# Optimization experiments

Hardware: AMD Instinct MI355X
Metric: run time of the kernel (lower is better)

## Reference

```python
import jax, jax.numpy as jnp
import numpy as np

N_NODES = 10000
N_EDGES = 320000
D = 256
L = 3
BN_EPS = 1e-5


def _segment_softmax(logits, seg, num_segments):
    # numerically stable softmax over variable-sized segments (incoming edges per node)
    m = jax.ops.segment_max(logits, seg, num_segments=num_segments)
    e = jnp.exp(logits - m[seg])
    s = jax.ops.segment_sum(e, seg, num_segments=num_segments)
    return e / s[seg]


def setup_inputs() -> dict:
    key = jax.random.key(0)
    ks = jax.random.split(key, 20)
    scale = 1.0 / np.sqrt(D)
    inp = {
        "x": jax.random.normal(ks[0], (N_NODES, D), dtype=jnp.float32),
        "edge_index": jax.random.randint(ks[1], (2, N_EDGES), 0, N_NODES, dtype=jnp.int64),
        # TransformerConv params (heads=1, concat=False)
        "Wq": jax.random.normal(ks[2], (D, D), jnp.float32) * scale,
        "bq": jnp.zeros((D,), jnp.float32),
        "Wk": jax.random.normal(ks[3], (D, D), jnp.float32) * scale,
        "bk": jnp.zeros((D,), jnp.float32),
        "Wv": jax.random.normal(ks[4], (D, D), jnp.float32) * scale,
        "bv": jnp.zeros((D,), jnp.float32),
        "Ws": jax.random.normal(ks[5], (D, D), jnp.float32) * scale,  # lin_skip (root weight)
        "bs": jnp.zeros((D,), jnp.float32),
        # SAGEConv params per layer: lin_l (neighbors, with bias), lin_r (root, no bias)
        "Wl": jax.random.normal(ks[6], (L, D, D), jnp.float32) * scale,
        "bl": jnp.zeros((L, D), jnp.float32),
        "Wr": jax.random.normal(ks[7], (L, D, D), jnp.float32) * scale,
        # BatchNorm affine params (eval mode: running_mean=0, running_var=1)
        "gamma": jnp.ones((L, D), jnp.float32) + 0.1 * jax.random.normal(ks[8], (L, D), jnp.float32),
        "beta": 0.1 * jax.random.normal(ks[9], (L, D), jnp.float32),
        # residual gate parameter (scalar)
        "alpha_res": jnp.asarray(0.5, jnp.float32),
    }
    return inp


def reference(x, edge_index, Wq, bq, Wk, bk, Wv, bv, Ws, bs, Wl, bl, Wr, gamma, beta, alpha_res):
    src, dst = edge_index[0], edge_index[1]  # message j -> i
    n, d = x.shape

    # ---- TransformerConv (heads=1, concat=False, eval: no dropout) ----
    q = x @ Wq + bq
    k = x @ Wk + bk
    v = x @ Wv + bv
    logits = jnp.sum(q[dst] * k[src], axis=-1) / jnp.sqrt(jnp.asarray(d, x.dtype))  # [E]
    attn = _segment_softmax(logits, dst, n)  # [E]
    agg = jax.ops.segment_sum(attn[:, None] * v[src], dst, num_segments=n)  # [N,D]
    h = agg + x @ Ws + bs  # root/skip connection
    h = jax.nn.relu(h)

    # in-degree for SAGE mean aggregation
    deg = jax.ops.segment_sum(jnp.ones((src.shape[0],), x.dtype), dst, num_segments=n)
    deg = jnp.maximum(deg, 1.0)[:, None]

    prev = h
    bn_scale = 1.0 / jnp.sqrt(1.0 + BN_EPS)  # eval-mode BN with running stats (0, 1)
    al = jax.nn.sigmoid(alpha_res)
    for i in range(Wl.shape[0]):
        mean_nb = jax.ops.segment_sum(h[src], dst, num_segments=n) / deg  # gather-mean-scatter
        z = mean_nb @ Wl[i] + bl[i] + h @ Wr[i]
        z = z * bn_scale * gamma[i] + beta[i]
        z = al * z + (1.0 - al) * prev
        h = jax.nn.relu(z)
        prev = h
    return h
```

## Files before the change

kernel.cpp:

```cpp
#include <hip/hip_runtime.h>
#include <hip/hip_bf16.h>

typedef unsigned short u16;
typedef unsigned int u32;
typedef unsigned char u8;
typedef __bf16 bf16x8 __attribute__((ext_vector_type(8)));
typedef float f32x4 __attribute__((ext_vector_type(4)));
typedef float f32x2 __attribute__((ext_vector_type(2)));

#define DIM 256
#define BN_SCALE 0.9999950000374997f

__device__ __forceinline__ float bf2f(u16 u) {
    union { unsigned u; float f; } c; c.u = ((unsigned)u) << 16; return c.f;
}
__device__ __forceinline__ u16 f2bf(float f) {
    union { float f; unsigned u; } c; c.f = f;
    unsigned u = c.u;
    unsigned r = (u + 0x7FFFu + ((u >> 16) & 1u)) >> 16;
    return (u16)r;
}
__device__ __forceinline__ float asf(unsigned u) {
    union { unsigned u; float f; } c; c.u = u; return c.f;
}
__device__ __forceinline__ void cvt8(int4 v, float* f) {
    unsigned a0 = (unsigned)v.x, a1 = (unsigned)v.y, a2 = (unsigned)v.z, a3 = (unsigned)v.w;
    f[0] = asf(a0 << 16); f[1] = asf(a0 & 0xFFFF0000u);
    f[2] = asf(a1 << 16); f[3] = asf(a1 & 0xFFFF0000u);
    f[4] = asf(a2 << 16); f[5] = asf(a2 & 0xFFFF0000u);
    f[6] = asf(a3 << 16); f[7] = asf(a3 & 0xFFFF0000u);
}
__device__ __forceinline__ void dec4(unsigned u, float* f) {
    f32x2 lo = __builtin_amdgcn_cvt_pk_f32_fp8((int)u, false);
    f32x2 hi = __builtin_amdgcn_cvt_pk_f32_fp8((int)u, true);
    f[0] = lo.x; f[1] = lo.y; f[2] = hi.x; f[3] = hi.y;
}
__device__ __forceinline__ unsigned pack4(float a, float b, float c, float d) {
    int u = __builtin_amdgcn_cvt_pk_fp8_f32(a, b, 0, false);
    u = __builtin_amdgcn_cvt_pk_fp8_f32(c, d, u, true);
    return (unsigned)u;
}
__device__ __forceinline__ void gl_lds16(const u16* g, u16* l) {
    __builtin_amdgcn_global_load_lds(
        (__attribute__((address_space(1))) const u32*)(const void*)g,
        (__attribute__((address_space(3))) u32*)(void*)l, 16, 0, 0);
}

__global__ void k_detect(const u16* __restrict__ xu, const long long* __restrict__ e64,
                         int* __restrict__ flags) {
    int lane = threadIdx.x;
    int plausible = 0;
#pragma unroll
    for (int j = 0; j < 4; ++j) {
        u16 u = xu[lane * 4 + j];
        int ex = (u >> 7) & 0xFF;
        plausible += (u == 0 || (ex >= 115 && ex <= 131)) ? 1 : 0;
    }
#pragma unroll
    for (int o = 32; o; o >>= 1) plausible += __shfl_xor(plausible, o, 64);
    long long hi = e64[lane] >> 32;
    unsigned long long b = __ballot(hi == 0);
    if (lane == 0) {
        flags[0] = (plausible >= 200) ? 1 : 0;
        flags[1] = (b == ~0ULL) ? 1 : 0;
    }
}

struct CvtDesc {
    const void* src[15];
    int cum[16];
};
__global__ void k_convert(CvtDesc d, const int* __restrict__ flags,
                          u16* __restrict__ arena, int total) {
    int i = blockIdx.x * 256 + threadIdx.x;
    if (i >= total) return;
    int t = 0;
    while (i >= d.cum[t + 1]) ++t;
    int j = i - d.cum[t];
    u16 v;
    if (flags[0]) v = ((const u16*)d.src[t])[j];
    else          v = f2bf(((const float*)d.src[t])[j]);
    arena[i] = v;
}

struct TDesc { const u16* src[12]; u16* dst[12]; };
__global__ __launch_bounds__(256) void k_transpose(TDesc td) {
    __shared__ u16 t[64][72];
    int m = blockIdx.x >> 4, tl = blockIdx.x & 15;
    int tr = (tl >> 2) * 64, tc = (tl & 3) * 64;
    const u16* S = td.src[m];
    u16* D = td.dst[m];
    int r = threadIdx.x >> 2, cs = (threadIdx.x & 3) * 16;
    *(int4*)&t[r][cs]     = *(const int4*)&S[(tr + r) * 256 + tc + cs];
    *(int4*)&t[r][cs + 8] = *(const int4*)&S[(tr + r) * 256 + tc + cs + 8];
    __syncthreads();
    u16 tmp[16];
#pragma unroll
    for (int j = 0; j < 16; ++j) tmp[j] = t[cs + j][r];
    *(int4*)&D[(tc + r) * 256 + tr + cs]     = *(int4*)&tmp[0];
    *(int4*)&D[(tc + r) * 256 + tr + cs + 8] = *(int4*)&tmp[8];
}

__global__ void k_edges(const int* __restrict__ ei32, const int* __restrict__ flags,
                        int* __restrict__ srcN, int* __restrict__ dstN,
                        int* __restrict__ deg, int E) {
    int e = blockIdx.x * 256 + threadIdx.x;
    if (e >= E) return;
    const long long* ei64 = (const long long*)ei32;
    int w64 = flags[1];
    int s = w64 ? (int)ei64[e]     : ei32[e];
    int d = w64 ? (int)ei64[E + e] : ei32[E + e];
    srcN[e] = s; dstN[e] = d;
    atomicAdd(&deg[d], 1);
}

__global__ __launch_bounds__(1024) void k_scan(const int* __restrict__ deg,
                                               int* __restrict__ offs,
                                               int* __restrict__ cursor, int N, int E) {
    __shared__ int s[1024];
    int t = threadIdx.x;
    int P = (N + 1023) >> 10;
    int base = t * P;
    int run = 0;
    for (int j = 0; j < P; ++j) { int idx = base + j; if (idx < N) run += deg[idx]; }
    s[t] = run;
    __syncthreads();
    int total = run;
    for (int off = 1; off < 1024; off <<= 1) {
        int v = 0;
        if (t >= off) v = s[t - off];
        __syncthreads();
        if (t >= off) s[t] += v;
        __syncthreads();
    }
    int r = s[t] - total;
    for (int j = 0; j < P; ++j) {
        int idx = base + j;
        if (idx < N) { offs[idx] = r; cursor[idx] = r; r += deg[idx]; }
    }
    if (t == 0) offs[N] = E;
}

__global__ void k_fill(const int* __restrict__ srcN, const int* __restrict__ dstN,
                       int* __restrict__ cursor, int* __restrict__ csr, int E) {
    int e = blockIdx.x * 256 + threadIdx.x;
    if (e < E) {
        int d = dstN[e];
        int pos = atomicAdd(&cursor[d], 1);
        csr[pos] = srcN[e];
    }
}

__global__ __launch_bounds__(256) void gemm_qkvs(
    const u16* __restrict__ x, const u16* __restrict__ WT,
    const u16* __restrict__ bias, u16* __restrict__ out, int M) {
    __shared__ __align__(16) u16 lds[16384];
    u16* As = lds;
    u16* Bs = lds + 8192;
    int tid = threadIdx.x, w = tid >> 6, lane = tid & 63;
    int l15 = lane & 15, quad = lane >> 4;
    int lr = lane >> 3, lc = lane & 7;
    int bm0 = blockIdx.x * 128, bn0 = blockIdx.y * 128;
    f32x4 acc[4][4];
#pragma unroll
    for (int a = 0; a < 4; ++a)
#pragma unroll
        for (int b = 0; b < 4; ++b) acc[a][b] = (f32x4){0.f, 0.f, 0.f, 0.f};

    for (int k0 = 0; k0 < 256; k0 += 64) {
#pragma unroll
        for (int j = 0; j < 4; ++j) {
            int ar = (w * 4 + j) * 8 + lr;
            int grow = bm0 + ar; if (grow >= M) grow = M - 1;
            gl_lds16(x + (size_t)grow * 256 + k0 + lc * 8, &As[(w * 4 + j) * 512]);
        }
#pragma unroll
        for (int j = 0; j < 4; ++j) {
            int nr = (w * 4 + j) * 8 + lr;
            gl_lds16(WT + (size_t)(bn0 + nr) * 256 + k0 + lc * 8, &Bs[(w * 4 + j) * 512]);
        }
        __syncthreads();
        int wm = w & 1, wn = w >> 1;
#pragma unroll
        for (int s = 0; s < 2; ++s) {
            bf16x8 a[4], b[4];
#pragma unroll
            for (int t = 0; t < 4; ++t)
                a[t] = *(const bf16x8*)&As[(wm * 64 + t * 16 + l15) * 64 + s * 32 + quad * 8];
#pragma unroll
            for (int t = 0; t < 4; ++t)
                b[t] = *(const bf16x8*)&Bs[(wn * 64 + t * 16 + l15) * 64 + s * 32 + quad * 8];
#pragma unroll
            for (int rt = 0; rt < 4; ++rt)
#pragma unroll
                for (int ct = 0; ct < 4; ++ct)
                    acc[rt][ct] = __builtin_amdgcn_mfma_f32_16x16x32_bf16(a[rt], b[ct], acc[rt][ct], 0, 0, 0);
        }
        __syncthreads();
    }
    int wm = w & 1, wn = w >> 1;
    u16* oL = lds + w * 4096;
#pragma unroll
    for (int rt = 0; rt < 4; ++rt)
#pragma unroll
        for (int ct = 0; ct < 4; ++ct) {
            int col = bn0 + wn * 64 + ct * 16 + l15;
            float bv = bf2f(bias[col]);
#pragma unroll
            for (int r = 0; r < 4; ++r)
                oL[(rt * 16 + quad * 4 + r) * 64 + ct * 16 + l15] = f2bf(acc[rt][ct][r] + bv);
        }
    __syncthreads();
#pragma unroll
    for (int j = 0; j < 8; ++j) {
        int orow = j * 8 + lr;
        int grow = bm0 + wm * 64 + orow;
        if (grow < M)
            *(int4*)&out[(size_t)grow * 1024 + bn0 + wn * 64 + lc * 8] = *(const int4*)&oL[orow * 64 + lc * 8];
    }
}

__global__ void k_pack8(const u16* __restrict__ qkvs, u8* __restrict__ kv8, int N) {
    int t = blockIdx.x * 256 + threadIdx.x;
    if (t >= N * 64) return;
    int i = t >> 6, s = t & 63;
    int4 v = *(const int4*)(qkvs + (size_t)i * 1024 + 256 + s * 8);
    float f[8]; cvt8(v, f);
    uint2 o;
    o.x = pack4(f[0], f[1], f[2], f[3]);
    o.y = pack4(f[4], f[5], f[6], f[7]);
    *(uint2*)(kv8 + (size_t)i * 512 + s * 8) = o;
}

__global__ __launch_bounds__(256) void k_attn(const u16* __restrict__ qkvs,
                                              const u8* __restrict__ kv8,
                                              const int* __restrict__ csr,
                                              const int* __restrict__ offs,
                                              u16* __restrict__ hb,
                                              u8* __restrict__ h8, int N) {
    int wv = threadIdx.x >> 6, lane = threadIdx.x & 63;
    int i = blockIdx.x * 4 + wv;
    if (i >= N) return;
    int sub = lane & 7;
    int e8 = lane >> 3;
    size_t row = (size_t)i * 1024;

    float qf[32];
    {
        const u16* qp = qkvs + row + sub * 32;
#pragma unroll
        for (int j = 0; j < 4; ++j) {
            int4 v = *(const int4*)(qp + j * 8);
            float t[8]; cvt8(v, t);
#pragma unroll
            for (int d = 0; d < 8; ++d) qf[j * 8 + d] = t[d] * 0.0625f;
        }
    }
    int e0 = offs[i], e1 = offs[i + 1];
    float m = -1e30f, denom = 0.f;
    float acc[32];
#pragma unroll
    for (int j = 0; j < 32; ++j) acc[j] = 0.f;

    for (int base = e0; base < e1; base += 8) {
        int e = base + e8;
        int sidx = csr[(e < e1) ? e : (e1 - 1)];
        const u8* kp = kv8 + (size_t)sidx * 512 + sub * 32;
        uint4 ka = *(const uint4*)kp;
        uint4 kb = *(const uint4*)(kp + 16);
        uint4 va = *(const uint4*)(kp + 256);
        uint4 vb = *(const uint4*)(kp + 272);
        unsigned kw[8] = {ka.x, ka.y, ka.z, ka.w, kb.x, kb.y, kb.z, kb.w};
        float p = 0.f;
#pragma unroll
        for (int j = 0; j < 8; ++j) {
            float t[4]; dec4(kw[j], t);
            p += qf[j * 4] * t[0] + qf[j * 4 + 1] * t[1] + qf[j * 4 + 2] * t[2] + qf[j * 4 + 3] * t[3];
        }
        p += __shfl_xor(p, 1, 64);
        p += __shfl_xor(p, 2, 64);
        p += __shfl_xor(p, 4, 64);
        if (e >= e1) p = -1e30f;
        float pm = p;
        pm = fmaxf(pm, __shfl_xor(pm, 8, 64));
        pm = fmaxf(pm, __shfl_xor(pm, 16, 64));
        pm = fmaxf(pm, __shfl_xor(pm, 32, 64));
        if (pm > m) {
            float sc = __expf(m - pm);
            denom *= sc;
#pragma unroll
            for (int j = 0; j < 32; ++j) acc[j] *= sc;
            m = pm;
        }
        float w = __expf(p - m);
        denom += w;
        unsigned vw[8] = {va.x, va.y, va.z, va.w, vb.x, vb.y, vb.z, vb.w};
#pragma unroll
        for (int j = 0; j < 8; ++j) {
            float t[4]; dec4(vw[j], t);
            acc[j * 4]     += w * t[0];
            acc[j * 4 + 1] += w * t[1];
            acc[j * 4 + 2] += w * t[2];
            acc[j * 4 + 3] += w * t[3];
        }
    }
    denom += __shfl_xor(denom, 8, 64);
    denom += __shfl_xor(denom, 16, 64);
    denom += __shfl_xor(denom, 32, 64);
    float inv = (denom > 0.f) ? 1.f / denom : 0.f;
#pragma unroll
    for (int j = 0; j < 32; ++j) {
        acc[j] += __shfl_xor(acc[j], 8, 64);
        acc[j] += __shfl_xor(acc[j], 16, 64);
        acc[j] += __shfl_xor(acc[j], 32, 64);
    }
    if (e8 == 0) {
        const u16* skp = qkvs + row + 768 + sub * 32;
        float h[32];
#pragma unroll
        for (int j = 0; j < 4; ++j) {
            int4 sv = *(const int4*)(skp + j * 8);
            float t[8]; cvt8(sv, t);
            u16 o[8];
#pragma unroll
            for (int d = 0; d < 8; ++d) {
                float hv = fmaxf(acc[j * 8 + d] * inv + t[d], 0.f);
                h[j * 8 + d] = hv;
                o[d] = f2bf(hv);
            }
            *(int4*)(hb + (size_t)i * 256 + sub * 32 + j * 8) = *(const int4*)o;
        }
        uint4 p0, p1;
        p0.x = pack4(h[0], h[1], h[2], h[3]);   p0.y = pack4(h[4], h[5], h[6], h[7]);
        p0.z = pack4(h[8], h[9], h[10], h[11]); p0.w = pack4(h[12], h[13], h[14], h[15]);
        p1.x = pack4(h[16], h[17], h[18], h[19]); p1.y = pack4(h[20], h[21], h[22], h[23]);
        p1.z = pack4(h[24], h[25], h[26], h[27]); p1.w = pack4(h[28], h[29], h[30], h[31]);
        *(uint4*)(h8 + (size_t)i * 256 + sub * 32) = p0;
        *(uint4*)(h8 + (size_t)i * 256 + sub * 32 + 16) = p1;
    }
}

__global__ __launch_bounds__(256) void k_agg(const u8* __restrict__ h8,
                                             const int* __restrict__ csr,
                                             const int* __restrict__ offs,
                                             u16* __restrict__ mean_out, int N) {
    int half = threadIdx.x >> 5, hl = threadIdx.x & 31;
    int i = blockIdx.x * 8 + half;
    if (i >= N) return;
    int e0 = offs[i], e1 = offs[i + 1];
    const u8* base = h8 + (unsigned)hl * 8;
    float acc[8];
#pragma unroll
    for (int d = 0; d < 8; ++d) acc[d] = 0.f;
    int e = e0;
    for (; e + 8 <= e1; e += 8) {
        uint2 r[8];
#pragma unroll
        for (int j = 0; j < 8; ++j)
            r[j] = *(const uint2*)(base + (size_t)csr[e + j] * 256);
#pragma unroll
        for (int j = 0; j < 8; ++j) {
            float f0[4], f1[4];
            dec4(r[j].x, f0); dec4(r[j].y, f1);
            acc[0] += f0[0]; acc[1] += f0[1]; acc[2] += f0[2]; acc[3] += f0[3];
            acc[4] += f1[0]; acc[5] += f1[1]; acc[6] += f1[2]; acc[7] += f1[3];
        }
    }
    for (; e < e1; ++e) {
        uint2 r0 = *(const uint2*)(base + (size_t)csr[e] * 256);
        float f0[4], f1[4];
        dec4(r0.x, f0); dec4(r0.y, f1);
        acc[0] += f0[0]; acc[1] += f0[1]; acc[2] += f0[2]; acc[3] += f0[3];
        acc[4] += f1[0]; acc[5] += f1[1]; acc[6] += f1[2]; acc[7] += f1[3];
    }
    int dg = e1 - e0; if (dg < 1) dg = 1;
    float inv = 1.f / (float)dg;
    u16 o16[8];
#pragma unroll
    for (int d = 0; d < 8; ++d) o16[d] = f2bf(acc[d] * inv);
    *(int4*)(mean_out + (size_t)i * 256 + (unsigned)hl * 8) = *(const int4*)o16;
}

__global__ __launch_bounds__(256) void gemm_sage(
    const u16* __restrict__ meanA, const u16* __restrict__ hin,
    const u16* __restrict__ WlT, const u16* __restrict__ WrT,
    const u16* __restrict__ bl, const u16* __restrict__ gamma,
    const u16* __restrict__ beta, const u16* __restrict__ alpha,
    u16* __restrict__ hout, u8* __restrict__ h8out, float* __restrict__ fout, int M) {
    __shared__ __align__(16) u16 lds[12288];
    u16* As = lds;
    u16* Bs = lds + 8192;
    int tid = threadIdx.x, w = tid >> 6, lane = tid & 63;
    int l15 = lane & 15, quad = lane >> 4;
    int lr = lane >> 3, lc = lane & 7;
    int bm0 = blockIdx.x * 128, n0 = blockIdx.y * 64;
    f32x4 acc[2][4];
#pragma unroll
    for (int a = 0; a < 2; ++a)
#pragma unroll
        for (int b = 0; b < 4; ++b) acc[a][b] = (f32x4){0.f, 0.f, 0.f, 0.f};

    for (int k0 = 0; k0 < 512; k0 += 64) {
        const u16* Asrc = (k0 < 256) ? meanA : hin;
        const u16* Bsrc = (k0 < 256) ? WlT : WrT;
        int kc = k0 & 255;
#pragma unroll
        for (int j = 0; j < 4; ++j) {
            int ar = (w * 4 + j) * 8 + lr;
            int grow = bm0 + ar; if (grow >= M) grow = M - 1;
            gl_lds16(Asrc + (size_t)grow * 256 + kc + lc * 8, &As[(w * 4 + j) * 512]);
        }
#pragma unroll
        for (int j = 0; j < 2; ++j) {
            int nr = (w * 2 + j) * 8 + lr;
            gl_lds16(Bsrc + (size_t)(n0 + nr) * 256 + kc + lc * 8, &Bs[(w * 2 + j) * 512]);
        }
        __syncthreads();
#pragma unroll
        for (int s = 0; s < 2; ++s) {
            bf16x8 a[2], b[4];
#pragma unroll
            for (int t = 0; t < 2; ++t)
                a[t] = *(const bf16x8*)&As[(w * 32 + t * 16 + l15) * 64 + s * 32 + quad * 8];
#pragma unroll
            for (int t = 0; t < 4; ++t)
                b[t] = *(const bf16x8*)&Bs[(t * 16 + l15) * 64 + s * 32 + quad * 8];
#pragma unroll
            for (int rt = 0; rt < 2; ++rt)
#pragma unroll
                for (int ct = 0; ct < 4; ++ct)
                    acc[rt][ct] = __builtin_amdgcn_mfma_f32_16x16x32_bf16(a[rt], b[ct], acc[rt][ct], 0, 0, 0);
        }
        __syncthreads();
    }

    float al = 1.f / (1.f + __expf(-bf2f(alpha[0])));
    float alc = 1.f - al;
    u16* oL = lds + w * 2048;
#pragma unroll
    for (int rt = 0; rt < 2; ++rt)
#pragma unroll
        for (int ct = 0; ct < 4; ++ct) {
            int col = n0 + ct * 16 + l15;
            float g  = bf2f(gamma[col]) * BN_SCALE;
            float be = bf2f(beta[col]);
            float bb = bf2f(bl[col]);
#pragma unroll
            for (int r = 0; r < 4; ++r) {
                int grow = bm0 + w * 32 + rt * 16 + quad * 4 + r;
                float z = (acc[rt][ct][r] + bb) * g + be;
                float prev = (grow < M) ? bf2f(hin[(size_t)grow * 256 + col]) : 0.f;
                z = al * z + alc * prev;
                z = fmaxf(z, 0.f);
                oL[(rt * 16 + quad * 4 + r) * 64 + ct * 16 + l15] = f2bf(z);
                if (fout && grow < M) fout[(size_t)grow * 256 + col] = z;
            }
        }
    __syncthreads();
#pragma unroll
    for (int j = 0; j < 4; ++j) {
        int orow = j * 8 + lr;
        int grow = bm0 + w * 32 + orow;
        if (grow < M) {
            int4 hv = *(const int4*)&oL[orow * 64 + lc * 8];
            *(int4*)&hout[(size_t)grow * 256 + n0 + lc * 8] = hv;
            float f[8]; cvt8(hv, f);
            uint2 o8;
            o8.x = pack4(f[0], f[1], f[2], f[3]);
            o8.y = pack4(f[4], f[5], f[6], f[7]);
            *(uint2*)(h8out + (size_t)grow * 256 + n0 + lc * 8) = o8;
        }
    }
}

extern "C" void kernel_launch(void* const* d_in, const int* in_sizes, int n_in,
                              void* d_out, int out_size, void* d_ws, size_t ws_size,
                              hipStream_t stream) {
    int N = in_sizes[0] / DIM;
    int E = in_sizes[1] / 2;
    int L = in_sizes[10] / (DIM * DIM);

    const int map[15] = {0, 2, 4, 6, 8, 10, 12, 3, 5, 7, 9, 11, 13, 14, 15};
    CvtDesc cd;
    cd.cum[0] = 0;
    for (int t = 0; t < 15; ++t) {
        cd.src[t] = d_in[map[t]];
        cd.cum[t + 1] = cd.cum[t] + in_sizes[map[t]];
    }
    int total = cd.cum[15];

    char* ws = (char*)d_ws;
    size_t off = 0;
    auto take = [&](size_t bytes) { size_t c = off; off = (off + bytes + 255) & ~255ULL; return c; };

    int* flags  = (int*)(ws + take(16));
    u16* arena  = (u16*)(ws + take((size_t)total * 2));
    u16* WT     = (u16*)(ws + take((size_t)(4 + 2 * L) * DIM * DIM * 2));
    int* srcN   = (int*)(ws + take((size_t)E * 4));
    int* dstN   = (int*)(ws + take((size_t)E * 4));
    int* csr    = (int*)(ws + take((size_t)E * 4));
    int* deg    = (int*)(ws + take((size_t)N * 4));
    int* offs   = (int*)(ws + take((size_t)(N + 1) * 4));
    int* cursor = (int*)(ws + take((size_t)N * 4));
    u16* hB0    = (u16*)(ws + take((size_t)N * DIM * 2));
    u8*  kv8    = (u8*)(ws + take((size_t)N * 512));
    u16* qkvsB  = (u16*)(ws + take((size_t)N * 1024 * 2));
    u16* meanB  = qkvsB;
    u16* hB1    = qkvsB + (size_t)N * DIM;
    u8*  h8     = (u8*)srcN;
    (void)ws_size; (void)n_in; (void)out_size;

    const u16* xb  = arena + cd.cum[0];
    const u16* Wqb = arena + cd.cum[1];
    const u16* Wkb = arena + cd.cum[2];
    const u16* Wvb = arena + cd.cum[3];
    const u16* Wsb = arena + cd.cum[4];
    const u16* Wlb = arena + cd.cum[5];
    const u16* Wrb = arena + cd.cum[6];
    const u16* biasF = arena + cd.cum[7];
    const u16* blb = arena + cd.cum[11];
    const u16* gmb = arena + cd.cum[12];
    const u16* btb = arena + cd.cum[13];
    const u16* alb = arena + cd.cum[14];

    k_detect<<<1, 64, 0, stream>>>((const u16*)d_in[0], (const long long*)d_in[1], flags);
    k_convert<<<(total + 255) / 256, 256, 0, stream>>>(cd, flags, arena, total);

    TDesc td;
    int nMat = 0;
    const u16* wsrc[4] = {Wqb, Wkb, Wvb, Wsb};
    for (int t = 0; t < 4; ++t) { td.src[nMat] = wsrc[t]; td.dst[nMat] = WT + (size_t)nMat * DIM * DIM; ++nMat; }
    for (int l = 0; l < L; ++l) { td.src[nMat] = Wlb + (size_t)l * DIM * DIM; td.dst[nMat] = WT + (size_t)nMat * DIM * DIM; ++nMat; }
    for (int l = 0; l < L; ++l) { td.src[nMat] = Wrb + (size_t)l * DIM * DIM; td.dst[nMat] = WT + (size_t)nMat * DIM * DIM; ++nMat; }
    k_transpose<<<nMat * 16, 256, 0, stream>>>(td);

    hipMemsetAsync(deg, 0, (size_t)N * 4, stream);
    int eb = (E + 255) / 256;
    k_edges<<<eb, 256, 0, stream>>>((const int*)d_in[1], flags, srcN, dstN, deg, E);
    k_scan<<<1, 1024, 0, stream>>>(deg, offs, cursor, N, E);
    k_fill<<<eb, 256, 0, stream>>>(srcN, dstN, cursor, csr, E);

    int Mb128 = (N + 127) / 128;
    gemm_qkvs<<<dim3(Mb128, 8), 256, 0, stream>>>(xb, WT, biasF, qkvsB, N);
    k_pack8<<<(N * 64 + 255) / 256, 256, 0, stream>>>(qkvsB, kv8, N);
    k_attn<<<(N + 3) / 4, 256, 0, stream>>>(qkvsB, kv8, csr, offs, hB0, h8, N);

    for (int l = 0; l < L; ++l) {
        const u16* hin = (l & 1) ? hB1 : hB0;
        u16* hout      = (l & 1) ? hB0 : hB1;
        float* fout = (l == L - 1) ? (float*)d_out : nullptr;
        k_agg<<<(N + 7) / 8, 256, 0, stream>>>(h8, csr, offs, meanB, N);
        gemm_sage<<<dim3(Mb128, 4), 256, 0, stream>>>(
            meanB, hin, WT + (size_t)(4 + l) * DIM * DIM, WT + (size_t)(4 + L + l) * DIM * DIM,
            blb + (size_t)l * DIM, gmb + (size_t)l * DIM, btb + (size_t)l * DIM,
            alb, hout, h8, fout, N);
    }
}
```

Before: 301.2 us.

## Fuse preprocessing kernels, pack fp8 in QKV GEMM epilogue, rework neighbor aggregation

Folds the dtype/width detection into every consumer kernel instead of a separate launch. The deg zeroing moves into the convert kernel and weight conversion into the transpose kernel. The fp8 K/V packing moves into the QKV GEMM epilogue, removing a pass over the QKV buffer. Edge ids are read directly from the input, dropping the srcN/dstN staging arrays. The mean-aggregation kernel now uses a 64-lane wave per node with 16-byte loads over 4 edges at a time, and the last SAGE layer skips the bf16 and fp8 h writes. Each kernel now repeats the cheap detection, and h8 gets its own buffer.

```diff
diff --git a/kernel.cpp b/kernel.cpp
--- a/kernel.cpp
+++ b/kernel.cpp
@@ -46,53 +46,77 @@
         (__attribute__((address_space(3))) u32*)(void*)l, 16, 0, 0);
 }
 
-__global__ void k_detect(const u16* __restrict__ xu, const long long* __restrict__ e64,
-                         int* __restrict__ flags) {
-    int lane = threadIdx.x;
-    int plausible = 0;
+__device__ __forceinline__ int2 detect_inline(const u16* __restrict__ xu,
+                                              const long long* __restrict__ e64) {
+    int lane = threadIdx.x & 63;
+    int pl = 0;
 #pragma unroll
     for (int j = 0; j < 4; ++j) {
         u16 u = xu[lane * 4 + j];
         int ex = (u >> 7) & 0xFF;
-        plausible += (u == 0 || (ex >= 115 && ex <= 131)) ? 1 : 0;
-    }
-#pragma unroll
-    for (int o = 32; o; o >>= 1) plausible += __shfl_xor(plausible, o, 64);
+        pl += (u == 0 || (ex >= 115 && ex <= 131)) ? 1 : 0;
+    }
+#pragma unroll
+    for (int o = 32; o; o >>= 1) pl += __shfl_xor(pl, o, 64);
     long long hi = e64[lane] >> 32;
     unsigned long long b = __ballot(hi == 0);
-    if (lane == 0) {
-        flags[0] = (plausible >= 200) ? 1 : 0;
-        flags[1] = (b == ~0ULL) ? 1 : 0;
-    }
-}
-
-struct CvtDesc {
-    const void* src[15];
-    int cum[16];
-};
-__global__ void k_convert(CvtDesc d, const int* __restrict__ flags,
-                          u16* __restrict__ arena, int total) {
+    int2 r; r.x = (pl >= 200) ? 1 : 0; r.y = (b == ~0ULL) ? 1 : 0;
+    return r;
+}
+
+struct CvtDesc { const void* src[9]; int cum[10]; };
+__global__ void k_convert(CvtDesc d, const u16* __restrict__ xu,
+                          const long long* __restrict__ e64,
+                          u16* __restrict__ arena, int total,
+                          int* __restrict__ deg, int N) {
+    int2 fl = detect_inline(xu, e64);
     int i = blockIdx.x * 256 + threadIdx.x;
+    if (i < N) deg[i] = 0;
     if (i >= total) return;
     int t = 0;
     while (i >= d.cum[t + 1]) ++t;
     int j = i - d.cum[t];
     u16 v;
-    if (flags[0]) v = ((const u16*)d.src[t])[j];
-    else          v = f2bf(((const float*)d.src[t])[j]);
+    if (fl.x) v = ((const u16*)d.src[t])[j];
+    else      v = f2bf(((const float*)d.src[t])[j]);
     arena[i] = v;
 }
 
-struct TDesc { const u16* src[12]; u16* dst[12]; };
-__global__ __launch_bounds__(256) void k_transpose(TDesc td) {
+struct TDesc { const void* base[3]; int L; };
+__global__ __launch_bounds__(256) void k_transpose(TDesc td, const void* w0,
+                                                   const void* w1, const void* w2,
+                                                   const void* w3,
+                                                   const u16* __restrict__ xu,
+                                                   const long long* __restrict__ e64,
+                                                   u16* __restrict__ WT) {
     __shared__ u16 t[64][72];
+    int2 fl = detect_inline(xu, e64);
     int m = blockIdx.x >> 4, tl = blockIdx.x & 15;
     int tr = (tl >> 2) * 64, tc = (tl & 3) * 64;
-    const u16* S = td.src[m];
-    u16* D = td.dst[m];
+    const void* S;
+    size_t eoff = 0;
+    if (m < 4)            S = (m == 0) ? w0 : (m == 1) ? w1 : (m == 2) ? w2 : w3;
+    else if (m < 4 + td.L) { S = td.base[1]; eoff = (size_t)(m - 4) * DIM * DIM; }
+    else                   { S = td.base[2]; eoff = (size_t)(m - 4 - td.L) * DIM * DIM; }
+    u16* D = WT + (size_t)m * DIM * DIM;
     int r = threadIdx.x >> 2, cs = (threadIdx.x & 3) * 16;
-    *(int4*)&t[r][cs]     = *(const int4*)&S[(tr + r) * 256 + tc + cs];
-    *(int4*)&t[r][cs + 8] = *(const int4*)&S[(tr + r) * 256 + tc + cs + 8];
+    size_t src_idx = eoff + (size_t)(tr + r) * 256 + tc + cs;
+    if (fl.x) {
+        const u16* S16 = (const u16*)S + src_idx;
+        *(int4*)&t[r][cs]     = *(const int4*)S16;
+        *(int4*)&t[r][cs + 8] = *(const int4*)(S16 + 8);
+    } else {
+        const float* SF = (const float*)S + src_idx;
+        u16 tmp[16];
+#pragma unroll
+        for (int q = 0; q < 4; ++q) {
+            float4 v = *(const float4*)(SF + q * 4);
+            tmp[q * 4] = f2bf(v.x); tmp[q * 4 + 1] = f2bf(v.y);
+            tmp[q * 4 + 2] = f2bf(v.z); tmp[q * 4 + 3] = f2bf(v.w);
+        }
+        *(int4*)&t[r][cs]     = *(const int4*)&tmp[0];
+        *(int4*)&t[r][cs + 8] = *(const int4*)&tmp[8];
+    }
     __syncthreads();
     u16 tmp[16];
 #pragma unroll
@@ -101,16 +125,13 @@
     *(int4*)&D[(tc + r) * 256 + tr + cs + 8] = *(int4*)&tmp[8];
 }
 
-__global__ void k_edges(const int* __restrict__ ei32, const int* __restrict__ flags,
-                        int* __restrict__ srcN, int* __restrict__ dstN,
+__global__ void k_edges(const int* __restrict__ ei32, const u16* __restrict__ xu,
                         int* __restrict__ deg, int E) {
+    int2 fl = detect_inline(xu, (const long long*)ei32);
     int e = blockIdx.x * 256 + threadIdx.x;
     if (e >= E) return;
     const long long* ei64 = (const long long*)ei32;
-    int w64 = flags[1];
-    int s = w64 ? (int)ei64[e]     : ei32[e];
-    int d = w64 ? (int)ei64[E + e] : ei32[E + e];
-    srcN[e] = s; dstN[e] = d;
+    int d = fl.y ? (int)ei64[E + e] : ei32[E + e];
     atomicAdd(&deg[d], 1);
 }
 
@@ -141,19 +162,22 @@
     if (t == 0) offs[N] = E;
 }
 
-__global__ void k_fill(const int* __restrict__ srcN, const int* __restrict__ dstN,
+__global__ void k_fill(const int* __restrict__ ei32, const u16* __restrict__ xu,
                        int* __restrict__ cursor, int* __restrict__ csr, int E) {
+    int2 fl = detect_inline(xu, (const long long*)ei32);
     int e = blockIdx.x * 256 + threadIdx.x;
-    if (e < E) {
-        int d = dstN[e];
-        int pos = atomicAdd(&cursor[d], 1);
-        csr[pos] = srcN[e];
-    }
+    if (e >= E) return;
+    const long long* ei64 = (const long long*)ei32;
+    int s = fl.y ? (int)ei64[e]     : ei32[e];
+    int d = fl.y ? (int)ei64[E + e] : ei32[E + e];
+    int pos = atomicAdd(&cursor[d], 1);
+    csr[pos] = s;
 }
 
 __global__ __launch_bounds__(256) void gemm_qkvs(
     const u16* __restrict__ x, const u16* __restrict__ WT,
-    const u16* __restrict__ bias, u16* __restrict__ out, int M) {
+    const u16* __restrict__ bias, u16* __restrict__ out,
+    u8* __restrict__ kv8, int M) {
     __shared__ __align__(16) u16 lds[16384];
     u16* As = lds;
     u16* Bs = lds + 8192;
@@ -211,25 +235,23 @@
                 oL[(rt * 16 + quad * 4 + r) * 64 + ct * 16 + l15] = f2bf(acc[rt][ct][r] + bv);
         }
     __syncthreads();
+    int c0 = bn0 + wn * 64 + lc * 8;
 #pragma unroll
     for (int j = 0; j < 8; ++j) {
         int orow = j * 8 + lr;
         int grow = bm0 + wm * 64 + orow;
-        if (grow < M)
-            *(int4*)&out[(size_t)grow * 1024 + bn0 + wn * 64 + lc * 8] = *(const int4*)&oL[orow * 64 + lc * 8];
-    }
-}
-
-__global__ void k_pack8(const u16* __restrict__ qkvs, u8* __restrict__ kv8, int N) {
-    int t = blockIdx.x * 256 + threadIdx.x;
-    if (t >= N * 64) return;
-    int i = t >> 6, s = t & 63;
-    int4 v = *(const int4*)(qkvs + (size_t)i * 1024 + 256 + s * 8);
-    float f[8]; cvt8(v, f);
-    uint2 o;
-    o.x = pack4(f[0], f[1], f[2], f[3]);
-    o.y = pack4(f[4], f[5], f[6], f[7]);
-    *(uint2*)(kv8 + (size_t)i * 512 + s * 8) = o;
+        if (grow < M) {
+            int4 hv = *(const int4*)&oL[orow * 64 + lc * 8];
+            *(int4*)&out[(size_t)grow * 1024 + c0] = hv;
+            if (c0 >= 256 && c0 < 768) {
+                float f[8]; cvt8(hv, f);
+                uint2 o8;
+                o8.x = pack4(f[0], f[1], f[2], f[3]);
+                o8.y = pack4(f[4], f[5], f[6], f[7]);
+                *(uint2*)(kv8 + (size_t)grow * 512 + (c0 - 256)) = o8;
+            }
+        }
+    }
 }
 
 __global__ __launch_bounds__(256) void k_attn(const u16* __restrict__ qkvs,
@@ -241,8 +263,7 @@
     int wv = threadIdx.x >> 6, lane = threadIdx.x & 63;
     int i = blockIdx.x * 4 + wv;
     if (i >= N) return;
-    int sub = lane & 7;
-    int e8 = lane >> 3;
+    int sub = lane & 7, e8 = lane >> 3;
     size_t row = (size_t)i * 1024;
 
     float qf[32];
@@ -344,41 +365,56 @@
                                              const int* __restrict__ csr,
                                              const int* __restrict__ offs,
                                              u16* __restrict__ mean_out, int N) {
-    int half = threadIdx.x >> 5, hl = threadIdx.x & 31;
-    int i = blockIdx.x * 8 + half;
+    int w = threadIdx.x >> 6, lane = threadIdx.x & 63;
+    int i = blockIdx.x * 4 + w;
     if (i >= N) return;
+    int g = lane >> 4, sub = lane & 15;
     int e0 = offs[i], e1 = offs[i + 1];
-    const u8* base = h8 + (unsigned)hl * 8;
-    float acc[8];
-#pragma unroll
-    for (int d = 0; d < 8; ++d) acc[d] = 0.f;
+    float acc[16];
+#pragma unroll
+    for (int d = 0; d < 16; ++d) acc[d] = 0.f;
     int e = e0;
     for (; e + 8 <= e1; e += 8) {
-        uint2 r[8];
-#pragma unroll
-        for (int j = 0; j < 8; ++j)
-            r[j] = *(const uint2*)(base + (size_t)csr[e + j] * 256);
-#pragma unroll
-        for (int j = 0; j < 8; ++j) {
-            float f0[4], f1[4];
-            dec4(r[j].x, f0); dec4(r[j].y, f1);
-            acc[0] += f0[0]; acc[1] += f0[1]; acc[2] += f0[2]; acc[3] += f0[3];
-            acc[4] += f1[0]; acc[5] += f1[1]; acc[6] += f1[2]; acc[7] += f1[3];
-        }
-    }
-    for (; e < e1; ++e) {
-        uint2 r0 = *(const uint2*)(base + (size_t)csr[e] * 256);
-        float f0[4], f1[4];
-        dec4(r0.x, f0); dec4(r0.y, f1);
-        acc[0] += f0[0]; acc[1] += f0[1]; acc[2] += f0[2]; acc[3] += f0[3];
-        acc[4] += f1[0]; acc[5] += f1[1]; acc[6] += f1[2]; acc[7] += f1[3];
-    }
-    int dg = e1 - e0; if (dg < 1) dg = 1;
-    float inv = 1.f / (float)dg;
-    u16 o16[8];
-#pragma unroll
-    for (int d = 0; d < 8; ++d) o16[d] = f2bf(acc[d] * inv);
-    *(int4*)(mean_out + (size_t)i * 256 + (unsigned)hl * 8) = *(const int4*)o16;
+        int s0 = csr[e + g], s1 = csr[e + 4 + g];
+        uint4 r0 = *(const uint4*)(h8 + (size_t)s0 * 256 + sub * 16);
+        uint4 r1 = *(const uint4*)(h8 + (size_t)s1 * 256 + sub * 16);
+        float f0[16], f1[16];
+        dec4(r0.x, f0); dec4(r0.y, f0 + 4); dec4(r0.z, f0 + 8); dec4(r0.w, f0 + 12);
+        dec4(r1.x, f1); dec4(r1.y, f1 + 4); dec4(r1.z, f1 + 8); dec4(r1.w, f1 + 12);
+#pragma unroll
+        for (int d = 0; d < 16; ++d) acc[d] += f0[d] + f1[d];
+    }
+    for (; e + 4 <= e1; e += 4) {
+        int s0 = csr[e + g];
+        uint4 r0 = *(const uint4*)(h8 + (size_t)s0 * 256 + sub * 16);
+        float f0[16];
+        dec4(r0.x, f0); dec4(r0.y, f0 + 4); dec4(r0.z, f0 + 8); dec4(r0.w, f0 + 12);
+#pragma unroll
+        for (int d = 0; d < 16; ++d) acc[d] += f0[d];
+    }
+    if (e + g < e1) {
+        int s0 = csr[e + g];
+        uint4 r0 = *(const uint4*)(h8 + (size_t)s0 * 256 + sub * 16);
+        float f0[16];
+        dec4(r0.x, f0); dec4(r0.y, f0 + 4); dec4(r0.z, f0 + 8); dec4(r0.w, f0 + 12);
+#pragma unroll
+        for (int d = 0; d < 16; ++d) acc[d] += f0[d];
+    }
+#pragma unroll
+    for (int d = 0; d < 16; ++d) {
+        acc[d] += __shfl_xor(acc[d], 16, 64);
+        acc[d] += __shfl_xor(acc[d], 32, 64);
+    }
+    if (g == 0) {
+        int dg = e1 - e0; if (dg < 1) dg = 1;
+        float inv = 1.f / (float)dg;
+        u16 o16[16];
+#pragma unroll
+        for (int d = 0; d < 16; ++d) o16[d] = f2bf(acc[d] * inv);
+        u16* dst = mean_out + (size_t)i * 256 + sub * 16;
+        *(int4*)dst = *(const int4*)&o16[0];
+        *(int4*)(dst + 8) = *(const int4*)&o16[8];
+    }
 }
 
 __global__ __launch_bounds__(256) void gemm_sage(
@@ -456,6 +492,7 @@
                 if (fout && grow < M) fout[(size_t)grow * 256 + col] = z;
             }
         }
+    if (!hout) return;
     __syncthreads();
 #pragma unroll
     for (int j = 0; j < 4; ++j) {
@@ -480,79 +517,68 @@
     int E = in_sizes[1] / 2;
     int L = in_sizes[10] / (DIM * DIM);
 
-    const int map[15] = {0, 2, 4, 6, 8, 10, 12, 3, 5, 7, 9, 11, 13, 14, 15};
+    const u16* xu = (const u16*)d_in[0];
+    const long long* e64 = (const long long*)d_in[1];
+
+    const int map9[9] = {0, 3, 5, 7, 9, 11, 13, 14, 15};
     CvtDesc cd;
     cd.cum[0] = 0;
-    for (int t = 0; t < 15; ++t) {
-        cd.src[t] = d_in[map[t]];
-        cd.cum[t + 1] = cd.cum[t] + in_sizes[map[t]];
-    }
-    int total = cd.cum[15];
+    for (int t = 0; t < 9; ++t) {
+        cd.src[t] = d_in[map9[t]];
+        cd.cum[t + 1] = cd.cum[t] + in_sizes[map9[t]];
+    }
+    int total = cd.cum[9];
 
     char* ws = (char*)d_ws;
     size_t off = 0;
     auto take = [&](size_t bytes) { size_t c = off; off = (off + bytes + 255) & ~255ULL; return c; };
 
-    int* flags  = (int*)(ws + take(16));
     u16* arena  = (u16*)(ws + take((size_t)total * 2));
     u16* WT     = (u16*)(ws + take((size_t)(4 + 2 * L) * DIM * DIM * 2));
-    int* srcN   = (int*)(ws + take((size_t)E * 4));
-    int* dstN   = (int*)(ws + take((size_t)E * 4));
     int* csr    = (int*)(ws + take((size_t)E * 4));
     int* deg    = (int*)(ws + take((size_t)N * 4));
     int* offs   = (int*)(ws + take((size_t)(N + 1) * 4));
     int* cursor = (int*)(ws + take((size_t)N * 4));
     u16* hB0    = (u16*)(ws + take((size_t)N * DIM * 2));
     u8*  kv8    = (u8*)(ws + take((size_t)N * 512));
+    u8*  h8     = (u8*)(ws + take((size_t)N * 256));
     u16* qkvsB  = (u16*)(ws + take((size_t)N * 1024 * 2));
     u16* meanB  = qkvsB;
     u16* hB1    = qkvsB + (size_t)N * DIM;
-    u8*  h8     = (u8*)srcN;
     (void)ws_size; (void)n_in; (void)out_size;
 
-    const u16* xb  = arena + cd.cum[0];
-    const u16* Wqb = arena + cd.cum[1];
-    const u16* Wkb = arena + cd.cum[2];
-    const u16* Wvb = arena + cd.cum[3];
-    const u16* Wsb = arena + cd.cum[4];
-    const u16* Wlb = arena + cd.cum[5];
-    const u16* Wrb = arena + cd.cum[6];
-    const u16* biasF = arena + cd.cum[7];
-    const u16* blb = arena + cd.cum[11];
-    const u16* gmb = arena + cd.cum[12];
-    const u16* btb = arena + cd.cum[13];
-    const u16* alb = arena + cd.cum[14];
-
-    k_detect<<<1, 64, 0, stream>>>((const u16*)d_in[0], (const long long*)d_in[1], flags);
-    k_convert<<<(total + 255) / 256, 256, 0, stream>>>(cd, flags, arena, total);
+    const u16* xb    = arena + cd.cum[0];
+    const u16* biasF = arena + cd.cum[1];
+    const u16* blb   = arena + cd.cum[5];
+    const u16* gmb   = arena + cd.cum[6];
+    const u16* btb   = arena + cd.cum[7];
+    const u16* alb   = arena + cd.cum[8];
+
+    k_convert<<<(total + 255) / 256, 256, 0, stream>>>(cd, xu, e64, arena, total, deg, N);
 
     TDesc td;
-    int nMat = 0;
-    const u16* wsrc[4] = {Wqb, Wkb, Wvb, Wsb};
-    for (int t = 0; t < 4; ++t) { td.src[nMat] = wsrc[t]; td.dst[nMat] = WT + (size_t)nMat * DIM * DIM; ++nMat; }
-    for (int l = 0; l < L; ++l) { td.src[nMat] = Wlb + (size_t)l * DIM * DIM; td.dst[nMat] = WT + (size_t)nMat * DIM * DIM; ++nMat; }
-    for (int l = 0; l < L; ++l) { td.src[nMat] = Wrb + (size_t)l * DIM * DIM; td.dst[nMat] = WT + (size_t)nMat * DIM * DIM; ++nMat; }
-    k_transpose<<<nMat * 16, 256, 0, stream>>>(td);
-
-    hipMemsetAsync(deg, 0, (size_t)N * 4, stream);
+    td.base[0] = nullptr; td.base[1] = d_in[10]; td.base[2] = d_in[12]; td.L = L;
+    k_transpose<<<(4 + 2 * L) * 16, 256, 0, stream>>>(td, d_in[2], d_in[4], d_in[6], d_in[8],
+                                                      xu, e64, WT);
+
     int eb = (E + 255) / 256;
-    k_edges<<<eb, 256, 0, stream>>>((const int*)d_in[1], flags, srcN, dstN, deg, E);
+    k_edges<<<eb, 256, 0, stream>>>((const int*)d_in[1], xu, deg, E);
     k_scan<<<1, 1024, 0, stream>>>(deg, offs, cursor, N, E);
-    k_fill<<<eb, 256, 0, stream>>>(srcN, dstN, cursor, csr, E);
+    k_fill<<<eb, 256, 0, stream>>>((const int*)d_in[1], xu, cursor, csr, E);
 
     int Mb128 = (N + 127) / 128;
-    gemm_qkvs<<<dim3(Mb128, 8), 256, 0, stream>>>(xb, WT, biasF, qkvsB, N);
-    k_pack8<<<(N * 64 + 255) / 256, 256, 0, stream>>>(qkvsB, kv8, N);
+    gemm_qkvs<<<dim3(Mb128, 8), 256, 0, stream>>>(xb, WT, biasF, qkvsB, kv8, N);
     k_attn<<<(N + 3) / 4, 256, 0, stream>>>(qkvsB, kv8, csr, offs, hB0, h8, N);
 
     for (int l = 0; l < L; ++l) {
         const u16* hin = (l & 1) ? hB1 : hB0;
-        u16* hout      = (l & 1) ? hB0 : hB1;
-        float* fout = (l == L - 1) ? (float*)d_out : nullptr;
-        k_agg<<<(N + 7) / 8, 256, 0, stream>>>(h8, csr, offs, meanB, N);
+        u16* hout      = (l == L - 1) ? nullptr : ((l & 1) ? hB0 : hB1);
+        u8*  h8o       = (l == L - 1) ? nullptr : h8;
+        float* fout    = (l == L - 1) ? (float*)d_out : nullptr;
+        k_agg<<<(N + 3) / 4, 256, 0, stream>>>(h8, csr, offs, meanB, N);
         gemm_sage<<<dim3(Mb128, 4), 256, 0, stream>>>(
             meanB, hin, WT + (size_t)(4 + l) * DIM * DIM, WT + (size_t)(4 + L + l) * DIM * DIM,
             blb + (size_t)l * DIM, gmb + (size_t)l * DIM, btb + (size_t)l * DIM,
-            alb, hout, h8, fout, N);
-    }
-}
+            alb, hout, h8o, fout, N);
+    }
+}
```

New measurement: 293.1 us. 2.7% less time.
